# Optimization experiments

Hardware: AMD Instinct MI355X
Metric: run time of the kernel (lower is better)

The kernel has to match this reference:

```python
import jax, jax.numpy as jnp
import numpy as np

NEG = -1e30  # log-space 'zero'
BLANK = 0


def setup_inputs() -> dict:
    key = jax.random.key(0)
    T, B, V, L = 1000, 32, 2048, 64
    k1, k2 = jax.random.split(key)
    acts = jax.random.normal(k1, (T, B, V), dtype=jnp.float32)
    # concatenated labels, one sequence of length L per example, blank=0 excluded
    labels = jax.random.randint(k2, (B * L,), 1, V, dtype=jnp.int32)
    act_lens = jnp.full((B,), T, dtype=jnp.int32)
    label_lens = jnp.full((B,), L, dtype=jnp.int32)
    return {"acts": acts, "labels": labels, "act_lens": act_lens, "label_lens": label_lens}


def _ctc_total_cost(acts, labels, act_lens, label_lens):
    # acts: (T, B, V) raw activations; warp-ctc applies softmax internally (blank=0).
    T, B, V = acts.shape
    L = labels.shape[0] // B  # uniform label length (sum(label_lens) == len(labels))
    S = 2 * L + 1
    labels2d = labels.reshape(B, L)
    # extended label sequence: blank, l1, blank, l2, ..., blank  -> (B, S)
    ext = jnp.zeros((B, S), dtype=jnp.int32).at[:, 1::2].set(labels2d)
    # transitions from s-2 allowed only for non-blank differing from ext[s-2]
    ext_m2 = jnp.concatenate([jnp.full((B, 2), -1, dtype=jnp.int32), ext[:, :-2]], axis=1)
    allow2 = (ext != BLANK) & (ext != ext_m2)  # (B, S)

    logp = jax.nn.log_softmax(acts, axis=-1)  # (T, B, V)
    # gather log-probs of extended labels: (T, B, S)
    lp_ext = jnp.take_along_axis(logp, jnp.broadcast_to(ext[None], (T, B, S)), axis=2)

    # alpha init at t=0: only s=0 (blank) and s=1 (first label)
    alpha0 = jnp.full((B, S), NEG, dtype=acts.dtype)
    alpha0 = alpha0.at[:, 0].set(lp_ext[0, :, 0]).at[:, 1].set(lp_ext[0, :, 1])

    def step(alpha, xs):
        t, lp_t = xs  # lp_t: (B, S)
        a1 = jnp.concatenate([jnp.full((B, 1), NEG, alpha.dtype), alpha[:, :-1]], axis=1)
        a2 = jnp.concatenate([jnp.full((B, 2), NEG, alpha.dtype), alpha[:, :-2]], axis=1)
        a2 = jnp.where(allow2, a2, NEG)
        new = jnp.logaddexp(jnp.logaddexp(alpha, a1), a2) + lp_t
        # freeze alpha for sequences that have already ended
        new = jnp.where((t < act_lens)[:, None], new, alpha)
        return new, None

    alphaT, _ = jax.lax.scan(step, alpha0, (jnp.arange(1, T), lp_ext[1:]))

    # terminal states: last blank (s=2*label_len) and last label (s=2*label_len-1)
    s_last = (2 * label_lens).astype(jnp.int32)  # (B,)
    a_end1 = jnp.take_along_axis(alphaT, s_last[:, None], axis=1)[:, 0]
    a_end2 = jnp.take_along_axis(alphaT, (s_last - 1)[:, None], axis=1)[:, 0]
    loss_b = -jnp.logaddexp(a_end1, a_end2)  # (B,)
    # size_average=False, length_average=False -> plain sum, returned as shape (1,)
    return jnp.sum(loss_b)[None]


def reference(acts, labels, act_lens, label_lens):
    return _ctc_total_cost(acts, labels, act_lens, label_lens)
```

## Files before the change

kernel.cpp:

```cpp
#include <hip/hip_runtime.h>
#include <stdint.h>

#define LOG2E  1.4426950408889634f
#define LN2    0.6931471805599453f
#define BIAS_E 32

typedef float v4f __attribute__((ext_vector_type(4)));

__device__ __forceinline__ float dpp_shr1_z(float x) {
  int r = __builtin_amdgcn_update_dpp(0, __float_as_int(x), 0x138, 0xf, 0xf, true);
  return __int_as_float(r);
}

template <int CTRL>
__device__ __forceinline__ float dpp_max(float v) {
  int r = __builtin_amdgcn_update_dpp(0, __float_as_int(v), CTRL, 0xf, 0xf, true);
  return fmaxf(v, __int_as_float(r));
}

__device__ __forceinline__ float wave_max_uniform(float v) {
  v = dpp_max<0x111>(v);
  v = dpp_max<0x112>(v);
  v = dpp_max<0x114>(v);
  v = dpp_max<0x118>(v);
  v = dpp_max<0x142>(v);
  v = dpp_max<0x143>(v);
  int gm = __builtin_amdgcn_readlane(__float_as_int(v), 63);
  return __int_as_float(gm);
}

__global__ __launch_bounds__(256) void k_prob_gather(
    const float* __restrict__ acts, const int* __restrict__ labels,
    float* __restrict__ lp, int T, int Tp, int B, int V, int L) {
  const int lane = threadIdx.x & 63;
  const uint32_t r = blockIdx.x * 4u + (threadIdx.x >> 6);
  if (r >= (uint32_t)(T * B)) return;
  const uint32_t b = r / (uint32_t)T;
  const uint32_t t = r % (uint32_t)T;
  const float* __restrict__ row = acts + ((size_t)t * (size_t)B + b) * (size_t)V;

  float mx, l2s;
  if (V == 2048) {
    const float4* row4 = (const float4*)row;
    float vals[32];
    mx = -3.0e38f;
#pragma unroll
    for (int q = 0; q < 8; ++q) {
      float4 v = row4[lane + (q << 6)];
      vals[q*4+0] = v.x; vals[q*4+1] = v.y; vals[q*4+2] = v.z; vals[q*4+3] = v.w;
      mx = fmaxf(mx, fmaxf(fmaxf(v.x, v.y), fmaxf(v.z, v.w)));
    }
#pragma unroll
    for (int off = 32; off >= 1; off >>= 1) mx = fmaxf(mx, __shfl_xor(mx, off, 64));
    float s = 0.0f;
#pragma unroll
    for (int k = 0; k < 32; ++k) s += exp2f((vals[k] - mx) * LOG2E);
#pragma unroll
    for (int off = 32; off >= 1; off >>= 1) s += __shfl_xor(s, off, 64);
    l2s = log2f(s);
  } else {
    float m = -3.0e38f, s = 0.0f;
    for (int i = lane; i < V; i += 64) {
      float x = row[i];
      float m2 = fmaxf(m, x);
      s = s * exp2f((m - m2) * LOG2E) + exp2f((x - m2) * LOG2E);
      m = m2;
    }
#pragma unroll
    for (int off = 32; off >= 1; off >>= 1) {
      float mo = __shfl_xor(m, off, 64), so = __shfl_xor(s, off, 64);
      float m2 = fmaxf(m, mo);
      s = s * exp2f((m - m2) * LOG2E) + so * exp2f((mo - m2) * LOG2E);
      m = m2;
    }
    mx = m;
    l2s = log2f(s);
  }

  float* __restrict__ out = lp + (size_t)b * (size_t)(L + 1) * (size_t)Tp;
  if (lane < L) {
    int lab = labels[b * (uint32_t)L + lane];
    out[(size_t)(1 + lane) * Tp + t] = exp2f((row[lab] - mx) * LOG2E - l2s);
  }
  if (lane == 0) out[t] = exp2f((row[0] - mx) * LOG2E - l2s);
}

__global__ __launch_bounds__(64, 1) void k_ctc_fwd(
    const float* __restrict__ lp, const int* __restrict__ labels,
    const int* __restrict__ act_lens, const int* __restrict__ label_lens,
    float* __restrict__ loss, int T, int Tp, int B, int L) {
  const int b = blockIdx.x;
  const int lane = threadIdx.x;
  const int Tact = __builtin_amdgcn_readfirstlane(min(act_lens[b], T));
  const int ll   = __builtin_amdgcn_readfirstlane(min(label_lens[b], L));

  const float* __restrict__ chb = lp + (size_t)b * (size_t)(L + 1) * (size_t)Tp;
  const int lclamp = (lane < L) ? lane : (L - 1);
  const float* __restrict__ chl = chb + (size_t)(1 + lclamp) * (size_t)Tp;

  int lab_i = (lane < L) ? labels[(size_t)b * L + lane] : 0;
  int lab_p = (lane >= 1 && lane - 1 < L) ? labels[(size_t)b * L + lane - 1] : -1;
  const bool allow2 = (lane >= 1) && (lab_i != 0) && (lab_i != lab_p);

  __shared__ float A_[132];

  v4f r0, r1, r2, r3;
  v4f d0, d1, d2, d3;
  float4 qb0, qb1, qb2, qb3;
  float4 nb0, nb1, nb2, nb3;
  int acc_e = 0;
  int pend_e = 0;
  float pend_sc = 1.0f;

  asm volatile("s_waitcnt vmcnt(0) lgkmcnt(0)" ::: "memory");
  __builtin_amdgcn_sched_barrier(0);

#define LOADR(tt) { int tc = (tt); if (tc > Tp - 16) tc = Tp - 16;           \
    const float* p_ = chl + tc;                                              \
    asm volatile("global_load_dwordx4 %0, %4, off\n\t"                       \
                 "global_load_dwordx4 %1, %4, off offset:16\n\t"             \
                 "global_load_dwordx4 %2, %4, off offset:32\n\t"             \
                 "global_load_dwordx4 %3, %4, off offset:48"                 \
                 : "=&v"(r0), "=&v"(r1), "=&v"(r2), "=&v"(r3) : "v"(p_)); }

#define WAITR asm volatile("s_waitcnt vmcnt(0)"                              \
                 : "+v"(r0), "+v"(r1), "+v"(r2), "+v"(r3));

#define COPYD { d0 = r0; d1 = r1; d2 = r2; d3 = r3; }

#define LOADB(D, tt) { int tc = (tt); if (tc > Tp - 16) tc = Tp - 16;        \
    const float4* pb4 = (const float4*)(chb + tc);                           \
    D##0 = pb4[0]; D##1 = pb4[1]; D##2 = pb4[2]; D##3 = pb4[3]; }

#define ST(PB, PL) { float pa = dpp_shr1_z(s1);                              \
    float cc = allow2 ? pa : 0.0f;                                           \
    float n0 = (s0 + pa) * (PB);                                             \
    float n1 = ((s0 + s1) + cc) * (PL);                                      \
    float n2 = (s2 + s1) * (PB);                                             \
    s0 = n0; s1 = n1; s2 = n2; }

#define RESC { s0 *= pend_sc; s1 *= pend_sc; s2 *= pend_sc; acc_e += pend_e; \
    float gm = wave_max_uniform(fmaxf(fmaxf(s0, s1), s2));                   \
    int e = ((__float_as_int(gm) >> 23) & 0xff) - 127 - BIAS_E;              \
    if (e < -126) e = -126;                                                  \
    pend_e = e;                                                              \
    pend_sc = __int_as_float((127 - e) << 23); }

#define STG(PB, PL, tt) { if ((tt) >= 1 && (tt) < Tact) ST(PB, PL) }

#define WIN16 {                                                              \
    ST(qb0.x, d0.x) ST(qb0.y, d0.y) ST(qb0.z, d0.z) ST(qb0.w, d0.w) RESC     \
    ST(qb1.x, d1.x) ST(qb1.y, d1.y) ST(qb1.z, d1.z) ST(qb1.w, d1.w) RESC     \
    ST(qb2.x, d2.x) ST(qb2.y, d2.y) ST(qb2.z, d2.z) ST(qb2.w, d2.w) RESC     \
    ST(qb3.x, d3.x) ST(qb3.y, d3.y) ST(qb3.z, d3.z) ST(qb3.w, d3.w) RESC }

#define WIN16G(tb) {                                                         \
    STG(qb0.x, d0.x, (tb)+0)  STG(qb0.y, d0.y, (tb)+1)                       \
    STG(qb0.z, d0.z, (tb)+2)  STG(qb0.w, d0.w, (tb)+3)  RESC                 \
    STG(qb1.x, d1.x, (tb)+4)  STG(qb1.y, d1.y, (tb)+5)                       \
    STG(qb1.z, d1.z, (tb)+6)  STG(qb1.w, d1.w, (tb)+7)  RESC                 \
    STG(qb2.x, d2.x, (tb)+8)  STG(qb2.y, d2.y, (tb)+9)                       \
    STG(qb2.z, d2.z, (tb)+10) STG(qb2.w, d2.w, (tb)+11) RESC                 \
    STG(qb3.x, d3.x, (tb)+12) STG(qb3.y, d3.y, (tb)+13)                      \
    STG(qb3.z, d3.z, (tb)+14) STG(qb3.w, d3.w, (tb)+15) RESC }

#define SWAPB { qb0 = nb0; qb1 = nb1; qb2 = nb2; qb3 = nb3; }

  LOADR(0)
  LOADB(qb, 0)
  LOADB(nb, 16)
  WAITR
  COPYD
  LOADR(16)

  float s0 = (lane == 0) ? qb0.x : 0.0f;
  float s1 = (lane == 0) ? d0.x  : 0.0f;
  float s2 = 0.0f;

  WIN16G(0)
  SWAPB LOADB(nb, 32)
  int t0 = 16;

  while (t0 + 16 <= Tact) {
    WAITR
    COPYD
    LOADR(t0 + 16)
    WIN16
    SWAPB LOADB(nb, t0 + 32)
    t0 += 16;
  }

  if (t0 < Tact) {
    WAITR
    COPYD
    WIN16G(t0)
  }

#undef LOADR
#undef WAITR
#undef COPYD
#undef LOADB
#undef ST
#undef RESC
#undef STG
#undef WIN16
#undef WIN16G
#undef SWAPB

  A_[2 * lane] = s0;
  A_[2 * lane + 1] = s1;
  if (lane == 63) A_[128] = s2;
  __syncthreads();
  if (lane == 0) {
    int sl = 2 * ll;
    float a1 = A_[sl];
    float a2 = (sl >= 1) ? A_[sl - 1] : 0.0f;
    loss[b] = -(logf(a1 + a2) + (float)acc_e * LN2);
  }
}

__global__ __launch_bounds__(64) void k_sum(const float* __restrict__ loss,
                                            float* __restrict__ out, int B) {
  int lane = threadIdx.x;
  float s = 0.0f;
  for (int i = lane; i < B; i += 64) s += loss[i];
#pragma unroll
  for (int off = 32; off >= 1; off >>= 1) s += __shfl_xor(s, off, 64);
  if (lane == 0) out[0] = s;
}

extern "C" void kernel_launch(void* const* d_in, const int* in_sizes, int n_in,
                              void* d_out, int out_size, void* d_ws, size_t ws_size,
                              hipStream_t stream) {
  const float* acts       = (const float*)d_in[0];
  const int*   labels     = (const int*)d_in[1];
  const int*   act_lens   = (const int*)d_in[2];
  const int*   label_lens = (const int*)d_in[3];

  const int B = in_sizes[2];
  const int L = in_sizes[1] / B;
  const int T = 1000;
  const int V = (int)((long long)in_sizes[0] / ((long long)T * (long long)B));
  const int Tp = (T + 31) & ~31;

  float* lp    = (float*)d_ws;
  float* lossb = lp + (size_t)B * (size_t)(L + 1) * (size_t)Tp;

  k_prob_gather<<<dim3((T * B + 3) / 4), dim3(256), 0, stream>>>(
      acts, labels, lp, T, Tp, B, V, L);
  k_ctc_fwd<<<dim3(B), dim3(64), 0, stream>>>(lp, labels, act_lens, label_lens,
                                              lossb, T, Tp, B, L);
  k_sum<<<dim3(1), dim3(64), 0, stream>>>(lossb, (float*)d_out, B);
}
```

Baseline: 121.0 us.

## Fuse softmax-gather and CTC recursion into one kernel with per-window counters

```diff
diff --git a/kernel.cpp b/kernel.cpp
--- a/kernel.cpp
+++ b/kernel.cpp
@@ -29,66 +29,80 @@
   return __int_as_float(gm);
 }
 
-__global__ __launch_bounds__(256) void k_prob_gather(
+__device__ __forceinline__ uint32_t ldcnt(const uint32_t* p) {
+  return __hip_atomic_load(p, __ATOMIC_RELAXED, __HIP_MEMORY_SCOPE_AGENT);
+}
+
+__global__ __launch_bounds__(256, 1) void k_fused(
     const float* __restrict__ acts, const int* __restrict__ labels,
-    float* __restrict__ lp, int T, int Tp, int B, int V, int L) {
-  const int lane = threadIdx.x & 63;
-  const uint32_t r = blockIdx.x * 4u + (threadIdx.x >> 6);
-  if (r >= (uint32_t)(T * B)) return;
-  const uint32_t b = r / (uint32_t)T;
-  const uint32_t t = r % (uint32_t)T;
-  const float* __restrict__ row = acts + ((size_t)t * (size_t)B + b) * (size_t)V;
-
-  float mx, l2s;
-  if (V == 2048) {
-    const float4* row4 = (const float4*)row;
-    float vals[32];
-    mx = -3.0e38f;
-#pragma unroll
-    for (int q = 0; q < 8; ++q) {
-      float4 v = row4[lane + (q << 6)];
-      vals[q*4+0] = v.x; vals[q*4+1] = v.y; vals[q*4+2] = v.z; vals[q*4+3] = v.w;
-      mx = fmaxf(mx, fmaxf(fmaxf(v.x, v.y), fmaxf(v.z, v.w)));
+    const int* __restrict__ act_lens, const int* __restrict__ label_lens,
+    float* __restrict__ lp, float* __restrict__ lossb, uint32_t* __restrict__ cnt,
+    int T, int Tp, int B, int V, int L, int PCH, int NW) {
+
+  __shared__ float A_[132];
+
+  if (blockIdx.x >= (uint32_t)B) {
+    const int g   = blockIdx.x - B;
+    const int pb  = g % B;
+    const int tch = g / B;
+    const int wv  = threadIdx.x >> 6;
+    const int lane = threadIdx.x & 63;
+    const int t = tch * 4 + wv;
+    if (t < T) {
+      const float* __restrict__ row = acts + ((size_t)t * (size_t)B + pb) * (size_t)V;
+      float mx, l2s;
+      if (V == 2048) {
+        const float4* row4 = (const float4*)row;
+        float vals[32];
+        mx = -3.0e38f;
+#pragma unroll
+        for (int q = 0; q < 8; ++q) {
+          float4 v = row4[lane + (q << 6)];
+          vals[q*4+0] = v.x; vals[q*4+1] = v.y; vals[q*4+2] = v.z; vals[q*4+3] = v.w;
+          mx = fmaxf(mx, fmaxf(fmaxf(v.x, v.y), fmaxf(v.z, v.w)));
+        }
+#pragma unroll
+        for (int off = 32; off >= 1; off >>= 1) mx = fmaxf(mx, __shfl_xor(mx, off, 64));
+        float s = 0.0f;
+#pragma unroll
+        for (int k = 0; k < 32; ++k) s += exp2f((vals[k] - mx) * LOG2E);
+#pragma unroll
+        for (int off = 32; off >= 1; off >>= 1) s += __shfl_xor(s, off, 64);
+        l2s = log2f(s);
+      } else {
+        float m = -3.0e38f, s = 0.0f;
+        for (int i = lane; i < V; i += 64) {
+          float x = row[i];
+          float m2 = fmaxf(m, x);
+          s = s * exp2f((m - m2) * LOG2E) + exp2f((x - m2) * LOG2E);
+          m = m2;
+        }
+#pragma unroll
+        for (int off = 32; off >= 1; off >>= 1) {
+          float mo = __shfl_xor(m, off, 64), so = __shfl_xor(s, off, 64);
+          float m2 = fmaxf(m, mo);
+          s = s * exp2f((m - m2) * LOG2E) + so * exp2f((mo - m2) * LOG2E);
+          m = m2;
+        }
+        mx = m;
+        l2s = log2f(s);
+      }
+      float* __restrict__ out = lp + (size_t)pb * (size_t)(L + 1) * (size_t)Tp;
+      if (lane < L) {
+        int lab = labels[pb * (uint32_t)L + lane];
+        out[(size_t)(1 + lane) * Tp + t] = exp2f((row[lab] - mx) * LOG2E - l2s);
+      }
+      if (lane == 0) out[t] = exp2f((row[0] - mx) * LOG2E - l2s);
     }
-#pragma unroll
-    for (int off = 32; off >= 1; off >>= 1) mx = fmaxf(mx, __shfl_xor(mx, off, 64));
-    float s = 0.0f;
-#pragma unroll
-    for (int k = 0; k < 32; ++k) s += exp2f((vals[k] - mx) * LOG2E);
-#pragma unroll
-    for (int off = 32; off >= 1; off >>= 1) s += __shfl_xor(s, off, 64);
-    l2s = log2f(s);
-  } else {
-    float m = -3.0e38f, s = 0.0f;
-    for (int i = lane; i < V; i += 64) {
-      float x = row[i];
-      float m2 = fmaxf(m, x);
-      s = s * exp2f((m - m2) * LOG2E) + exp2f((x - m2) * LOG2E);
-      m = m2;
+    __syncthreads();
+    if (threadIdx.x == 0) {
+      __threadfence();
+      atomicAdd(&cnt[(size_t)pb * 64 + (tch >> 2)], 1u);
     }
-#pragma unroll
-    for (int off = 32; off >= 1; off >>= 1) {
-      float mo = __shfl_xor(m, off, 64), so = __shfl_xor(s, off, 64);
-      float m2 = fmaxf(m, mo);
-      s = s * exp2f((m - m2) * LOG2E) + so * exp2f((mo - m2) * LOG2E);
-      m = m2;
-    }
-    mx = m;
-    l2s = log2f(s);
-  }
-
-  float* __restrict__ out = lp + (size_t)b * (size_t)(L + 1) * (size_t)Tp;
-  if (lane < L) {
-    int lab = labels[b * (uint32_t)L + lane];
-    out[(size_t)(1 + lane) * Tp + t] = exp2f((row[lab] - mx) * LOG2E - l2s);
-  }
-  if (lane == 0) out[t] = exp2f((row[0] - mx) * LOG2E - l2s);
-}
-
-__global__ __launch_bounds__(64, 1) void k_ctc_fwd(
-    const float* __restrict__ lp, const int* __restrict__ labels,
-    const int* __restrict__ act_lens, const int* __restrict__ label_lens,
-    float* __restrict__ loss, int T, int Tp, int B, int L) {
+    return;
+  }
+
+  if (threadIdx.x >= 64) return;
   const int b = blockIdx.x;
   const int lane = threadIdx.x;
   const int Tact = __builtin_amdgcn_readfirstlane(min(act_lens[b], T));
@@ -97,12 +111,12 @@
   const float* __restrict__ chb = lp + (size_t)b * (size_t)(L + 1) * (size_t)Tp;
   const int lclamp = (lane < L) ? lane : (L - 1);
   const float* __restrict__ chl = chb + (size_t)(1 + lclamp) * (size_t)Tp;
+  const uint32_t* cb = cnt + (size_t)b * 64;
+  const int wlast = NW - 1;
 
   int lab_i = (lane < L) ? labels[(size_t)b * L + lane] : 0;
   int lab_p = (lane >= 1 && lane - 1 < L) ? labels[(size_t)b * L + lane - 1] : -1;
   const bool allow2 = (lane >= 1) && (lab_i != 0) && (lab_i != lab_p);
-
-  __shared__ float A_[132];
 
   v4f r0, r1, r2, r3;
   v4f d0, d1, d2, d3;
@@ -111,6 +125,9 @@
   int acc_e = 0;
   int pend_e = 0;
   float pend_sc = 1.0f;
+
+#define TGTW(w) ((uint32_t)(((PCH - 4*(w)) >= 4) ? 4 : (PCH - 4*(w))))
+#define POLLW(w) { while (ldcnt(cb + (w)) < TGTW(w)) __builtin_amdgcn_s_sleep(8); }
 
   asm volatile("s_waitcnt vmcnt(0) lgkmcnt(0)" ::: "memory");
   __builtin_amdgcn_sched_barrier(0);
@@ -166,6 +183,11 @@
 
 #define SWAPB { qb0 = nb0; qb1 = nb1; qb2 = nb2; qb3 = nb3; }
 
+  POLLW(0)
+  { int w_ = (1 < wlast) ? 1 : wlast; POLLW(w_) }
+  { int w_ = (2 < wlast) ? 2 : wlast; POLLW(w_) }
+  __threadfence();
+
   LOADR(0)
   LOADB(qb, 0)
   LOADB(nb, 16)
@@ -179,14 +201,25 @@
 
   WIN16G(0)
   SWAPB LOADB(nb, 32)
+  uint32_t cv1 = ldcnt(cb + ((2 < wlast) ? 2 : wlast));
+  uint32_t cv2 = ldcnt(cb + ((3 < wlast) ? 3 : wlast));
   int t0 = 16;
 
   while (t0 + 16 <= Tact) {
     WAITR
     COPYD
-    LOADR(t0 + 16)
-    WIN16
-    SWAPB LOADB(nb, t0 + 32)
+    { const int w = t0 >> 4;
+      const int w1 = (w + 1 < wlast) ? w + 1 : wlast;
+      const int w2 = (w + 2 < wlast) ? w + 2 : wlast;
+      if (cv1 < TGTW(w1)) POLLW(w1)
+      if (cv2 < TGTW(w2)) POLLW(w2)
+      __threadfence();
+      LOADR(t0 + 16)
+      WIN16
+      SWAPB LOADB(nb, t0 + 32)
+      cv1 = ldcnt(cb + ((w + 2 < wlast) ? w + 2 : wlast));
+      cv2 = ldcnt(cb + ((w + 3 < wlast) ? w + 3 : wlast));
+    }
     t0 += 16;
   }
 
@@ -206,16 +239,18 @@
 #undef WIN16
 #undef WIN16G
 #undef SWAPB
+#undef TGTW
+#undef POLLW
 
   A_[2 * lane] = s0;
   A_[2 * lane + 1] = s1;
   if (lane == 63) A_[128] = s2;
-  __syncthreads();
+  __builtin_amdgcn_sched_barrier(0);
   if (lane == 0) {
     int sl = 2 * ll;
     float a1 = A_[sl];
     float a2 = (sl >= 1) ? A_[sl - 1] : 0.0f;
-    loss[b] = -(logf(a1 + a2) + (float)acc_e * LN2);
+    lossb[b] = -(logf(a1 + a2) + (float)acc_e * LN2);
   }
 }
 
@@ -241,14 +276,16 @@
   const int L = in_sizes[1] / B;
   const int T = 1000;
   const int V = (int)((long long)in_sizes[0] / ((long long)T * (long long)B));
-  const int Tp = (T + 31) & ~31;
-
-  float* lp    = (float*)d_ws;
-  float* lossb = lp + (size_t)B * (size_t)(L + 1) * (size_t)Tp;
-
-  k_prob_gather<<<dim3((T * B + 3) / 4), dim3(256), 0, stream>>>(
-      acts, labels, lp, T, Tp, B, V, L);
-  k_ctc_fwd<<<dim3(B), dim3(64), 0, stream>>>(lp, labels, act_lens, label_lens,
-                                              lossb, T, Tp, B, L);
+  const int Tp  = (T + 31) & ~31;
+  const int PCH = (T + 3) / 4;
+  const int NW  = (T + 15) / 16;
+
+  float*    lp    = (float*)d_ws;
+  float*    lossb = lp + (size_t)B * (size_t)(L + 1) * (size_t)Tp;
+  uint32_t* cnt   = (uint32_t*)(lossb + B);
+
+  hipMemsetAsync(cnt, 0, (size_t)B * 64 * sizeof(uint32_t), stream);
+  k_fused<<<dim3(B + B * PCH), dim3(256), 0, stream>>>(
+      acts, labels, act_lens, label_lens, lp, lossb, cnt, T, Tp, B, V, L, PCH, NW);
   k_sum<<<dim3(1), dim3(64), 0, stream>>>(lossb, (float*)d_out, B);
 }
```

New measurement: 477.8 us. 295% more time.

## Tile gathered probabilities into per-16-step window blocks and drop inline-asm loads

Applied to the files above, without the earlier changes.

```diff
diff --git a/kernel.cpp b/kernel.cpp
--- a/kernel.cpp
+++ b/kernel.cpp
@@ -4,8 +4,6 @@
 #define LOG2E  1.4426950408889634f
 #define LN2    0.6931471805599453f
 #define BIAS_E 32
-
-typedef float v4f __attribute__((ext_vector_type(4)));
 
 __device__ __forceinline__ float dpp_shr1_z(float x) {
   int r = __builtin_amdgcn_update_dpp(0, __float_as_int(x), 0x138, 0xf, 0xf, true);
@@ -31,7 +29,7 @@
 
 __global__ __launch_bounds__(256) void k_prob_gather(
     const float* __restrict__ acts, const int* __restrict__ labels,
-    float* __restrict__ lp, int T, int Tp, int B, int V, int L) {
+    float* __restrict__ lp, int T, int NWB, int B, int V, int L) {
   const int lane = threadIdx.x & 63;
   const uint32_t r = blockIdx.x * 4u + (threadIdx.x >> 6);
   if (r >= (uint32_t)(T * B)) return;
@@ -77,26 +75,29 @@
     l2s = log2f(s);
   }
 
-  float* __restrict__ out = lp + (size_t)b * (size_t)(L + 1) * (size_t)Tp;
+  const int w = (int)(t >> 4), k = (int)(t & 15);
+  const size_t WBLK = (size_t)(L + 1) * 16;
+  float* __restrict__ out = lp + ((size_t)b * (size_t)NWB + (size_t)w) * WBLK;
   if (lane < L) {
     int lab = labels[b * (uint32_t)L + lane];
-    out[(size_t)(1 + lane) * Tp + t] = exp2f((row[lab] - mx) * LOG2E - l2s);
-  }
-  if (lane == 0) out[t] = exp2f((row[0] - mx) * LOG2E - l2s);
+    out[(size_t)(1 + lane) * 16 + k] = exp2f((row[lab] - mx) * LOG2E - l2s);
+  }
+  if (lane == 0) out[k] = exp2f((row[0] - mx) * LOG2E - l2s);
 }
 
 __global__ __launch_bounds__(64, 1) void k_ctc_fwd(
     const float* __restrict__ lp, const int* __restrict__ labels,
     const int* __restrict__ act_lens, const int* __restrict__ label_lens,
-    float* __restrict__ loss, int T, int Tp, int B, int L) {
+    float* __restrict__ loss, int T, int NWB, int B, int L) {
   const int b = blockIdx.x;
   const int lane = threadIdx.x;
   const int Tact = __builtin_amdgcn_readfirstlane(min(act_lens[b], T));
   const int ll   = __builtin_amdgcn_readfirstlane(min(label_lens[b], L));
 
-  const float* __restrict__ chb = lp + (size_t)b * (size_t)(L + 1) * (size_t)Tp;
+  const size_t WBLK = (size_t)(L + 1) * 16;
+  const float* __restrict__ chblk = lp + (size_t)b * (size_t)NWB * WBLK;
   const int lclamp = (lane < L) ? lane : (L - 1);
-  const float* __restrict__ chl = chb + (size_t)(1 + lclamp) * (size_t)Tp;
+  const int wmax = NWB - 1;
 
   int lab_i = (lane < L) ? labels[(size_t)b * L + lane] : 0;
   int lab_p = (lane >= 1 && lane - 1 < L) ? labels[(size_t)b * L + lane - 1] : -1;
@@ -104,33 +105,22 @@
 
   __shared__ float A_[132];
 
-  v4f r0, r1, r2, r3;
-  v4f d0, d1, d2, d3;
+  float4 ql0, ql1, ql2, ql3;
+  float4 nl0, nl1, nl2, nl3;
   float4 qb0, qb1, qb2, qb3;
   float4 nb0, nb1, nb2, nb3;
   int acc_e = 0;
   int pend_e = 0;
   float pend_sc = 1.0f;
 
-  asm volatile("s_waitcnt vmcnt(0) lgkmcnt(0)" ::: "memory");
-  __builtin_amdgcn_sched_barrier(0);
-
-#define LOADR(tt) { int tc = (tt); if (tc > Tp - 16) tc = Tp - 16;           \
-    const float* p_ = chl + tc;                                              \
-    asm volatile("global_load_dwordx4 %0, %4, off\n\t"                       \
-                 "global_load_dwordx4 %1, %4, off offset:16\n\t"             \
-                 "global_load_dwordx4 %2, %4, off offset:32\n\t"             \
-                 "global_load_dwordx4 %3, %4, off offset:48"                 \
-                 : "=&v"(r0), "=&v"(r1), "=&v"(r2), "=&v"(r3) : "v"(p_)); }
-
-#define WAITR asm volatile("s_waitcnt vmcnt(0)"                              \
-                 : "+v"(r0), "+v"(r1), "+v"(r2), "+v"(r3));
-
-#define COPYD { d0 = r0; d1 = r1; d2 = r2; d3 = r3; }
-
-#define LOADB(D, tt) { int tc = (tt); if (tc > Tp - 16) tc = Tp - 16;        \
-    const float4* pb4 = (const float4*)(chb + tc);                           \
-    D##0 = pb4[0]; D##1 = pb4[1]; D##2 = pb4[2]; D##3 = pb4[3]; }
+#define LOADL(D, wc) { int w_ = (wc); if (w_ > wmax) w_ = wmax;              \
+    const float4* p4 = (const float4*)(chblk + (size_t)w_ * WBLK             \
+                                       + (size_t)(1 + lclamp) * 16);         \
+    D##0 = p4[0]; D##1 = p4[1]; D##2 = p4[2]; D##3 = p4[3]; }
+
+#define LOADB(D, wc) { int w_ = (wc); if (w_ > wmax) w_ = wmax;              \
+    const float4* p4 = (const float4*)(chblk + (size_t)w_ * WBLK);           \
+    D##0 = p4[0]; D##1 = p4[1]; D##2 = p4[2]; D##3 = p4[3]; }
 
 #define ST(PB, PL) { float pa = dpp_shr1_z(s1);                              \
     float cc = allow2 ? pa : 0.0f;                                           \
@@ -149,63 +139,56 @@
 #define STG(PB, PL, tt) { if ((tt) >= 1 && (tt) < Tact) ST(PB, PL) }
 
 #define WIN16 {                                                              \
-    ST(qb0.x, d0.x) ST(qb0.y, d0.y) ST(qb0.z, d0.z) ST(qb0.w, d0.w) RESC     \
-    ST(qb1.x, d1.x) ST(qb1.y, d1.y) ST(qb1.z, d1.z) ST(qb1.w, d1.w) RESC     \
-    ST(qb2.x, d2.x) ST(qb2.y, d2.y) ST(qb2.z, d2.z) ST(qb2.w, d2.w) RESC     \
-    ST(qb3.x, d3.x) ST(qb3.y, d3.y) ST(qb3.z, d3.z) ST(qb3.w, d3.w) RESC }
+    ST(qb0.x, ql0.x) ST(qb0.y, ql0.y) ST(qb0.z, ql0.z) ST(qb0.w, ql0.w) RESC \
+    ST(qb1.x, ql1.x) ST(qb1.y, ql1.y) ST(qb1.z, ql1.z) ST(qb1.w, ql1.w) RESC \
+    ST(qb2.x, ql2.x) ST(qb2.y, ql2.y) ST(qb2.z, ql2.z) ST(qb2.w, ql2.w) RESC \
+    ST(qb3.x, ql3.x) ST(qb3.y, ql3.y) ST(qb3.z, ql3.z) ST(qb3.w, ql3.w) RESC }
 
 #define WIN16G(tb) {                                                         \
-    STG(qb0.x, d0.x, (tb)+0)  STG(qb0.y, d0.y, (tb)+1)                       \
-    STG(qb0.z, d0.z, (tb)+2)  STG(qb0.w, d0.w, (tb)+3)  RESC                 \
-    STG(qb1.x, d1.x, (tb)+4)  STG(qb1.y, d1.y, (tb)+5)                       \
-    STG(qb1.z, d1.z, (tb)+6)  STG(qb1.w, d1.w, (tb)+7)  RESC                 \
-    STG(qb2.x, d2.x, (tb)+8)  STG(qb2.y, d2.y, (tb)+9)                       \
-    STG(qb2.z, d2.z, (tb)+10) STG(qb2.w, d2.w, (tb)+11) RESC                 \
-    STG(qb3.x, d3.x, (tb)+12) STG(qb3.y, d3.y, (tb)+13)                      \
-    STG(qb3.z, d3.z, (tb)+14) STG(qb3.w, d3.w, (tb)+15) RESC }
-
-#define SWAPB { qb0 = nb0; qb1 = nb1; qb2 = nb2; qb3 = nb3; }
-
-  LOADR(0)
-  LOADB(qb, 0)
-  LOADB(nb, 16)
-  WAITR
-  COPYD
-  LOADR(16)
+    STG(qb0.x, ql0.x, (tb)+0)  STG(qb0.y, ql0.y, (tb)+1)                     \
+    STG(qb0.z, ql0.z, (tb)+2)  STG(qb0.w, ql0.w, (tb)+3)  RESC               \
+    STG(qb1.x, ql1.x, (tb)+4)  STG(qb1.y, ql1.y, (tb)+5)                     \
+    STG(qb1.z, ql1.z, (tb)+6)  STG(qb1.w, ql1.w, (tb)+7)  RESC               \
+    STG(qb2.x, ql2.x, (tb)+8)  STG(qb2.y, ql2.y, (tb)+9)                     \
+    STG(qb2.z, ql2.z, (tb)+10) STG(qb2.w, ql2.w, (tb)+11) RESC               \
+    STG(qb3.x, ql3.x, (tb)+12) STG(qb3.y, ql3.y, (tb)+13)                    \
+    STG(qb3.z, ql3.z, (tb)+14) STG(qb3.w, ql3.w, (tb)+15) RESC }
+
+#define SWAPQ { ql0 = nl0; ql1 = nl1; ql2 = nl2; ql3 = nl3;                  \
+                qb0 = nb0; qb1 = nb1; qb2 = nb2; qb3 = nb3; }
+
+  LOADL(ql, 0) LOADB(qb, 0)
+  LOADL(nl, 1) LOADB(nb, 1)
 
   float s0 = (lane == 0) ? qb0.x : 0.0f;
-  float s1 = (lane == 0) ? d0.x  : 0.0f;
+  float s1 = (lane == 0) ? ql0.x : 0.0f;
   float s2 = 0.0f;
 
   WIN16G(0)
-  SWAPB LOADB(nb, 32)
   int t0 = 16;
 
   while (t0 + 16 <= Tact) {
-    WAITR
-    COPYD
-    LOADR(t0 + 16)
+    const int w = t0 >> 4;
+    SWAPQ
+    LOADL(nl, w + 1)
+    LOADB(nb, w + 1)
     WIN16
-    SWAPB LOADB(nb, t0 + 32)
     t0 += 16;
   }
 
   if (t0 < Tact) {
-    WAITR
-    COPYD
+    SWAPQ
     WIN16G(t0)
   }
 
-#undef LOADR
-#undef WAITR
-#undef COPYD
+#undef LOADL
 #undef LOADB
 #undef ST
 #undef RESC
 #undef STG
 #undef WIN16
 #undef WIN16G
-#undef SWAPB
+#undef SWAPQ
 
   A_[2 * lane] = s0;
   A_[2 * lane + 1] = s1;
@@ -241,14 +224,14 @@
   const int L = in_sizes[1] / B;
   const int T = 1000;
   const int V = (int)((long long)in_sizes[0] / ((long long)T * (long long)B));
-  const int Tp = (T + 31) & ~31;
+  const int NWB = ((T + 15) / 16 + 3) & ~3;
 
   float* lp    = (float*)d_ws;
-  float* lossb = lp + (size_t)B * (size_t)(L + 1) * (size_t)Tp;
+  float* lossb = lp + (size_t)B * (size_t)NWB * (size_t)(L + 1) * 16;
 
   k_prob_gather<<<dim3((T * B + 3) / 4), dim3(256), 0, stream>>>(
-      acts, labels, lp, T, Tp, B, V, L);
+      acts, labels, lp, T, NWB, B, V, L);
   k_ctc_fwd<<<dim3(B), dim3(64), 0, stream>>>(lp, labels, act_lens, label_lens,
-                                              lossb, T, Tp, B, L);
+                                              lossb, T, NWB, B, L);
   k_sum<<<dim3(1), dim3(64), 0, stream>>>(lossb, (float*)d_out, B);
 }
```

New measurement: 112.3 us, median of 2. 1.08x faster.
